# Optimization experiments

Measured on AMD Instinct MI355X. Metric: run time of the kernel, lower is better.

The kernel has to match this reference:

```python
import jax, jax.numpy as jnp
import numpy as np

N_LAYERS = 2
D_MODEL = 768
D_INNER = 1536
D_STATE = 16
D_CONV = 4
DT_RANK = 48
VOCAB = 50257
EPS = 1e-5


def _rms(x, w):
    return x * jax.lax.rsqrt(jnp.mean(x * x, axis=-1, keepdims=True) + EPS) * w


def _mixer(x, in_w, cw, cb, xp_w, dt_w, dt_b, a_log, d_skip, out_w):
    b, l, _ = x.shape
    xz = x @ in_w.T                                  # (b,l,2*d_in)
    u, z = jnp.split(xz, 2, axis=-1)                 # each (b,l,d_in)
    # causal depthwise conv1d
    uc = jax.lax.conv_general_dilated(
        u.transpose(0, 2, 1), cw[:, None, :], (1,), [(D_CONV - 1, 0)],
        feature_group_count=D_INNER, dimension_numbers=("NCH", "OIH", "NCH"))
    u = jax.nn.silu((uc + cb[:, None]).transpose(0, 2, 1))
    x_dbl = u @ xp_w.T                               # (b,l,dt_rank+2n)
    dt, B, C = jnp.split(x_dbl, [DT_RANK, DT_RANK + D_STATE], axis=-1)
    delta = jax.nn.softplus(dt @ dt_w.T + dt_b)      # (b,l,d_in)
    A = -jnp.exp(a_log)                              # (d_in,n)
    dA = jnp.exp(delta[..., None] * A)               # (b,l,d_in,n)
    dBu = delta[..., None] * B[:, :, None, :] * u[..., None]

    def step(h, inp):
        dA_t, dBu_t, C_t = inp
        h = dA_t * h + dBu_t
        return h, jnp.einsum("bdn,bn->bd", h, C_t)

    h0 = jnp.zeros((b, D_INNER, D_STATE), x.dtype)
    _, ys = jax.lax.scan(step, h0, (dA.transpose(1, 0, 2, 3),
                                    dBu.transpose(1, 0, 2, 3),
                                    C.transpose(1, 0, 2)))
    y = ys.transpose(1, 0, 2) + u * d_skip           # (b,l,d_in)
    y = y * jax.nn.silu(z)
    return y @ out_w.T


def setup_inputs() -> dict:
    key = jax.random.key(0)
    ks = jax.random.split(key, 12)
    std = 0.02
    emb = jax.random.normal(ks[0], (VOCAB, D_MODEL), jnp.float32) * std
    emb = emb.at[0].set(0.0)  # padding_idx=0
    tokens = jax.random.randint(ks[1], (2, 1024), 0, VOCAB)
    a_log = jnp.tile(jnp.log(jnp.arange(1, D_STATE + 1, dtype=jnp.float32)),
                     (N_LAYERS, D_INNER, 1))
    return {
        "tokens": tokens,
        "emb": emb,
        "norm_w": jnp.ones((N_LAYERS, D_MODEL), jnp.float32),
        "in_proj_w": jax.random.normal(ks[2], (N_LAYERS, 2 * D_INNER, D_MODEL), jnp.float32) * std,
        "conv_w": jax.random.normal(ks[3], (N_LAYERS, D_INNER, D_CONV), jnp.float32) * 0.1,
        "conv_b": jnp.zeros((N_LAYERS, D_INNER), jnp.float32),
        "x_proj_w": jax.random.normal(ks[4], (N_LAYERS, DT_RANK + 2 * D_STATE, D_INNER), jnp.float32) * std,
        "dt_proj_w": jax.random.normal(ks[5], (N_LAYERS, D_INNER, DT_RANK), jnp.float32) * (DT_RANK ** -0.5),
        "dt_proj_b": jax.random.uniform(ks[6], (N_LAYERS, D_INNER), jnp.float32, -4.6, -2.0),
        "A_log": a_log,
        "D": jnp.ones((N_LAYERS, D_INNER), jnp.float32),
        "out_proj_w": jax.random.normal(ks[7], (N_LAYERS, D_MODEL, D_INNER), jnp.float32) * (std / np.sqrt(2 * N_LAYERS)),
        "normf_w": jnp.ones((D_MODEL,), jnp.float32),
        "lm_head_w": jax.random.normal(ks[8], (VOCAB, D_MODEL), jnp.float32) * std,
    }


def reference(tokens, emb, norm_w, in_proj_w, conv_w, conv_b, x_proj_w,
              dt_proj_w, dt_proj_b, A_log, D, out_proj_w, normf_w, lm_head_w):
    x = emb[tokens]                                  # (b,l,d_model)
    for i in range(N_LAYERS):
        x = x + _mixer(_rms(x, norm_w[i]), in_proj_w[i], conv_w[i], conv_b[i],
                       x_proj_w[i], dt_proj_w[i], dt_proj_b[i], A_log[i],
                       D[i], out_proj_w[i])
    x = _rms(x, normf_w)
    return x @ lm_head_w.T                           # (b,l,vocab)
```

## Files before the change

### kernel.cpp

```cpp
#include <hip/hip_runtime.h>
#include <hip/hip_bf16.h>
#include <math.h>

#define DM 768
#define DI 1536
#define DSN 16
#define NB 2
#define SL 1024
#define MROWS 2048
#define VOC 50257
#define VOCP 50432
#define EPSR 1e-5f

typedef __attribute__((ext_vector_type(8))) short short8;
typedef __attribute__((ext_vector_type(4))) float f32x4;
typedef __attribute__((ext_vector_type(4))) unsigned short us4;
typedef unsigned short u16;

__device__ inline u16 f2bf(float f) {
    unsigned u = __builtin_bit_cast(unsigned, f);
    u += 0x7FFFu + ((u >> 16) & 1u);
    return (u16)(u >> 16);
}

#define G_LDS16(g, l) __builtin_amdgcn_global_load_lds( \
    (const __attribute__((address_space(1))) void*)(g), \
    (__attribute__((address_space(3))) void*)(l), 16, 0, 0)

__global__ __launch_bounds__(256)
void k_embed_rms(const int* __restrict__ tok, const float* __restrict__ emb,
                 const float* __restrict__ w, float* __restrict__ x,
                 u16* __restrict__ out) {
    int r = blockIdx.x;
    int t = tok[r];
    const float* src = emb + (size_t)t * DM;
    int c0 = threadIdx.x * 3;
    float v[3]; float ss = 0.f;
#pragma unroll
    for (int i = 0; i < 3; ++i) {
        v[i] = src[c0 + i]; ss += v[i] * v[i];
        x[(size_t)r * DM + c0 + i] = v[i];
    }
#pragma unroll
    for (int o = 32; o > 0; o >>= 1) ss += __shfl_down(ss, o);
    __shared__ float s[4];
    int lane = threadIdx.x & 63, wv = threadIdx.x >> 6;
    if (lane == 0) s[wv] = ss;
    __syncthreads();
    float sc = rsqrtf((s[0] + s[1] + s[2] + s[3]) / (float)DM + EPSR);
#pragma unroll
    for (int i = 0; i < 3; ++i)
        out[(size_t)r * DM + c0 + i] = f2bf(v[i] * sc * w[c0 + i]);
}

__global__ __launch_bounds__(256)
void k_rmsnorm_bf16(const float* __restrict__ x, const float* __restrict__ w,
                    u16* __restrict__ out) {
    int r = blockIdx.x;
    const float* row = x + (size_t)r * DM;
    int c0 = threadIdx.x * 3;
    float v[3]; float ss = 0.f;
#pragma unroll
    for (int i = 0; i < 3; ++i) { v[i] = row[c0 + i]; ss += v[i] * v[i]; }
#pragma unroll
    for (int o = 32; o > 0; o >>= 1) ss += __shfl_down(ss, o);
    __shared__ float s[4];
    int lane = threadIdx.x & 63, wv = threadIdx.x >> 6;
    if (lane == 0) s[wv] = ss;
    __syncthreads();
    float sc = rsqrtf((s[0] + s[1] + s[2] + s[3]) / (float)DM + EPSR);
#pragma unroll
    for (int i = 0; i < 3; ++i)
        out[(size_t)r * DM + c0 + i] = f2bf(v[i] * sc * w[c0 + i]);
}

struct CvtSeg { const float* src; u16* dst; int sr, sc, sld, dc, blk0, total4; };
struct CvtArgs { CvtSeg seg[9]; };

__global__ __launch_bounds__(256)
void k_cvt_multi(CvtArgs a) {
    int b = blockIdx.x;
    int s = 0;
#pragma unroll
    for (int q = 1; q < 9; ++q) if (a.seg[q].blk0 <= b) s = q;
    const CvtSeg& g = a.seg[s];
    long i4 = (long)(b - g.blk0) * 256 + threadIdx.x;
    if (i4 >= g.total4) return;
    long i = i4 * 4;
    int r = (int)(i / g.dc), c0 = (int)(i % g.dc);
    us4 o;
#pragma unroll
    for (int e = 0; e < 4; ++e) {
        int c = c0 + e;
        float v = (r < g.sr && c < g.sc) ? g.src[(size_t)r * g.sld + c] : 0.f;
        o[e] = f2bf(v);
    }
    *(us4*)&g.dst[i] = o;
}

__global__ void k_cvt_pad4(const float* __restrict__ src, u16* __restrict__ dst,
                           int sr, int sc, int sld, int dc, long total4) {
    long i4 = (long)blockIdx.x * 256 + threadIdx.x;
    if (i4 >= total4) return;
    long i = i4 * 4;
    int r = (int)(i / dc), c0 = (int)(i % dc);
    us4 o;
#pragma unroll
    for (int e = 0; e < 4; ++e) {
        int c = c0 + e;
        float v = (r < sr && c < sc) ? src[(size_t)r * sld + c] : 0.f;
        o[e] = f2bf(v);
    }
    *(us4*)&dst[i] = o;
}

__global__ void k_conv_silu(const float* __restrict__ xz, const float* __restrict__ cw,
                            const float* __restrict__ cb, float* __restrict__ uc,
                            u16* __restrict__ ucb) {
    int d = blockIdx.x * 256 + threadIdx.x;
    int r = blockIdx.y;
    int l = r & (SL - 1);
    float acc = cb[d];
#pragma unroll
    for (int j = 0; j < 4; ++j) {
        int ls = l - 3 + j;
        if (ls >= 0) acc += xz[(size_t)(r - 3 + j) * (2 * DI) + d] * cw[d * 4 + j];
    }
    float s = acc / (1.f + __expf(-acc));
    uc[(size_t)r * DI + d] = s;
    ucb[(size_t)r * DI + d] = f2bf(s);
}

__global__ __launch_bounds__(512)
void k_scan2(const float* __restrict__ delta, const float* __restrict__ uc,
             const float* __restrict__ xdbl, const float* __restrict__ xz,
             const float* __restrict__ alog, const float* __restrict__ Dp,
             u16* __restrict__ ybf) {
    __shared__ float ds2[8][16][20], us2[8][16][20], bn2[8][16][20], cn2[8][16][20];
    __shared__ float Sm[8][16][16], Pm[8][16][16];
    int b  = blockIdx.x / 96;
    int d0 = (blockIdx.x % 96) * 16;
    int tid = threadIdx.x, w = tid >> 6, lane = tid & 63;
    int ch = lane >> 2, nq = lane & 3;
    int d = d0 + ch;
    float A[4];
#pragma unroll
    for (int k = 0; k < 4; ++k) A[k] = -__expf(alog[d * DSN + nq + 4 * k]);
    int tb = w * 128;

    float h[4] = {0.f, 0.f, 0.f, 0.f};
    float sdl = 0.f;
    for (int t0 = 0; t0 < 128; t0 += 16) {
        int row0 = b * SL + tb + t0;
#pragma unroll
        for (int i = 0; i < 4; ++i) {
            int lin = i * 64 + lane, tt = lin >> 4, cc = lin & 15;
            size_t row = (size_t)(row0 + tt);
            ds2[w][cc][tt] = delta[row * DI + d0 + cc];
            us2[w][cc][tt] = uc[row * DI + d0 + cc];
            bn2[w][cc][tt] = xdbl[row * 128 + 48 + cc];
        }
#pragma unroll
        for (int g4 = 0; g4 < 4; ++g4) {
            f32x4 dl = *(const f32x4*)&ds2[w][ch][g4 * 4];
            f32x4 uv = *(const f32x4*)&us2[w][ch][g4 * 4];
            f32x4 bv[4];
#pragma unroll
            for (int k = 0; k < 4; ++k) bv[k] = *(const f32x4*)&bn2[w][nq + 4 * k][g4 * 4];
#pragma unroll
            for (int s = 0; s < 4; ++s) {
                float du = dl[s] * uv[s];
                sdl += dl[s];
#pragma unroll
                for (int k = 0; k < 4; ++k) {
                    float dA = __expf(dl[s] * A[k]);
                    h[k] = h[k] * dA + du * bv[k][s];
                }
            }
        }
    }
#pragma unroll
    for (int k = 0; k < 4; ++k) {
        Sm[w][ch][nq + 4 * k] = h[k];
        Pm[w][ch][nq + 4 * k] = __expf(A[k] * sdl);
    }
    __syncthreads();
    if (tid < 256) {
        int c2 = tid >> 4, n2 = tid & 15;
        float H = 0.f;
#pragma unroll
        for (int g = 0; g < 8; ++g) {
            float hi = H;
            H = Pm[g][c2][n2] * H + Sm[g][c2][n2];
            Sm[g][c2][n2] = hi;
        }
    }
    __syncthreads();
    float Dv = Dp[d];
#pragma unroll
    for (int k = 0; k < 4; ++k) h[k] = Sm[w][ch][nq + 4 * k];
    for (int t0 = 0; t0 < 128; t0 += 16) {
        int row0 = b * SL + tb + t0;
#pragma unroll
        for (int i = 0; i < 4; ++i) {
            int lin = i * 64 + lane, tt = lin >> 4, cc = lin & 15;
            size_t row = (size_t)(row0 + tt);
            ds2[w][cc][tt] = delta[row * DI + d0 + cc];
            us2[w][cc][tt] = uc[row * DI + d0 + cc];
            bn2[w][cc][tt] = xdbl[row * 128 + 48 + cc];
            cn2[w][cc][tt] = xdbl[row * 128 + 64 + cc];
        }
#pragma unroll
        for (int g4 = 0; g4 < 4; ++g4) {
            f32x4 dl = *(const f32x4*)&ds2[w][ch][g4 * 4];
            f32x4 uv = *(const f32x4*)&us2[w][ch][g4 * 4];
            f32x4 bv[4], cv[4];
#pragma unroll
            for (int k = 0; k < 4; ++k) {
                bv[k] = *(const f32x4*)&bn2[w][nq + 4 * k][g4 * 4];
                cv[k] = *(const f32x4*)&cn2[w][nq + 4 * k][g4 * 4];
            }
#pragma unroll
            for (int s = 0; s < 4; ++s) {
                float du = dl[s] * uv[s];
                float p = 0.f;
#pragma unroll
                for (int k = 0; k < 4; ++k) {
                    float dA = __expf(dl[s] * A[k]);
                    h[k] = h[k] * dA + du * bv[k][s];
                    p += h[k] * cv[k][s];
                }
                p += __shfl_xor(p, 1);
                p += __shfl_xor(p, 2);
                if (nq == 0) {
                    size_t row = (size_t)(row0 + g4 * 4 + s);
                    float z = xz[row * (2 * DI) + DI + d];
                    float y = p + uv[s] * Dv;
                    y *= z / (1.f + __expf(-z));
                    ybf[row * DI + d] = f2bf(y);
                }
            }
        }
    }
}

template <int EPIL>
__global__ __launch_bounds__(256)
void k_gemm_bt(const u16* __restrict__ A, const u16* __restrict__ W,
               float* C, const float* RES,
               const float* __restrict__ BIASV,
               int K, int ldc, int nTm) {
    __shared__ u16 Al[128 * 32];
    __shared__ u16 Wl[128 * 32];
    int nwg = gridDim.x;
    int qc = nwg >> 3, rc = nwg & 7;
    int xcd = blockIdx.x & 7, j = blockIdx.x >> 3;
    int wg = (xcd < rc ? xcd * (qc + 1) : rc * (qc + 1) + (xcd - rc) * qc) + j;
    int m0 = (wg % nTm) * 128, n0 = (wg / nTm) * 128;

    int tid = threadIdx.x, wave = tid >> 6, lane = tid & 63;
    int wm = wave >> 1, wn = wave & 1;
    f32x4 acc[4][4] = {};
    const int rS = (lane >> 2);
    const int kS = (((lane & 3) ^ ((lane >> 3) & 3)) * 8);
    const int kofs = (((lane >> 4) ^ ((lane >> 1) & 3)) * 8);
    const int fr = lane & 15;

    for (int k0 = 0; k0 < K; k0 += 32) {
#pragma unroll
        for (int i = 0; i < 2; ++i) {
            int rowA = m0 + wave * 32 + i * 16 + rS;
            G_LDS16(A + (size_t)rowA * K + k0 + kS, &Al[wave * 1024 + i * 512]);
            int rowW = n0 + wave * 32 + i * 16 + rS;
            G_LDS16(W + (size_t)rowW * K + k0 + kS, &Wl[wave * 1024 + i * 512]);
        }
        __syncthreads();
        short8 af[4], bfr[4];
#pragma unroll
        for (int f = 0; f < 4; ++f) {
            af[f]  = *(const short8*)&Al[(wm * 64 + f * 16 + fr) * 32 + kofs];
            bfr[f] = *(const short8*)&Wl[(wn * 64 + f * 16 + fr) * 32 + kofs];
        }
#pragma unroll
        for (int i = 0; i < 4; ++i)
#pragma unroll
            for (int jj = 0; jj < 4; ++jj)
                acc[i][jj] = __builtin_amdgcn_mfma_f32_16x16x32_bf16(af[i], bfr[jj], acc[i][jj], 0, 0, 0);
        __syncthreads();
    }
    int r4 = (lane >> 4) * 4;
#pragma unroll
    for (int i = 0; i < 4; ++i)
#pragma unroll
        for (int jj = 0; jj < 4; ++jj) {
            int col = n0 + wn * 64 + jj * 16 + fr;
            float bia = (EPIL == 2) ? BIASV[col] : 0.f;
#pragma unroll
            for (int rr = 0; rr < 4; ++rr) {
                int row = m0 + wm * 64 + i * 16 + r4 + rr;
                size_t off = (size_t)row * ldc + col;
                float v = acc[i][jj][rr];
                if (EPIL == 1) v += RES[off];
                if (EPIL == 2) { v += bia; v = (v > 20.f) ? v : log1pf(__expf(v)); }
                C[off] = v;
            }
        }
}

#define BAR  __builtin_amdgcn_s_barrier()
#define LGK0 do { asm volatile("s_waitcnt lgkmcnt(0)" ::: "memory"); \
                  __builtin_amdgcn_sched_barrier(0); } while (0)
#define VMC3 asm volatile("s_waitcnt vmcnt(3)" ::: "memory")
#define VMC0 asm volatile("s_waitcnt vmcnt(0)" ::: "memory")

#define STAGE1(t, op, half, GB, RB) do {                                      \
    const u16* _g = (GB) + (size_t)((RB) + (half) * 128 + (w << 4) + srow) * K \
                    + (t) * 32 + scol;                                         \
    G_LDS16(_g, &lds[(t) & 1][op][half][w << 9]);                              \
} while (0)

#define RDA(dst, t, mq) do {                                                   \
    _Pragma("unroll") for (int _m = 0; _m < 4; ++_m)                           \
        dst[_m] = *(const short8*)&lds[(t) & 1][0][wm]                         \
            [((mq) * 64 + _m * 16 + fr) * 32 + rd_sw];                         \
} while (0)

#define RDB(t, nq) do {                                                       \
    _Pragma("unroll") for (int _n = 0; _n < 2; ++_n)                           \
        bfv[_n] = *(const short8*)&lds[(t) & 1][1][wbh]                        \
            [(wbr * 64 + (nq) * 32 + _n * 16 + fr) * 32 + rd_sw];              \
} while (0)

#define MM8(AF, mq, nq) do {                                                  \
    __builtin_amdgcn_s_setprio(1);                                            \
    _Pragma("unroll") for (int _m = 0; _m < 4; ++_m)                           \
    _Pragma("unroll") for (int _n = 0; _n < 2; ++_n)                           \
        acc[(mq) * 4 + _m][(nq) * 2 + _n] =                                    \
            __builtin_amdgcn_mfma_f32_16x16x32_bf16(                           \
                AF[_m], bfv[_n], acc[(mq) * 4 + _m][(nq) * 2 + _n], 0, 0, 0);  \
    __builtin_amdgcn_s_setprio(0);                                            \
} while (0)

template <int K>
__global__ __launch_bounds__(512, 2)
void k_gemm256(const u16* __restrict__ Ap, const u16* __restrict__ Wp,
               float* __restrict__ C, int ldc, int nmax, int nTm) {
    constexpr int NT = K / 32;
    constexpr int NI = NT / 2;
    __shared__ __align__(16) u16 lds[2][2][2][4096];

    int per8 = gridDim.x >> 3;
    int wg = (blockIdx.x & 7) * per8 + (blockIdx.x >> 3);
    int m0 = (wg % nTm) * 256, n0 = (wg / nTm) * 256;

    int tid = threadIdx.x, w = tid >> 6, lane = tid & 63;
    int wm = w >> 2, wn = w & 3, wbh = wn >> 1, wbr = wn & 1;
    int fr = lane & 15;
    int rd_sw = (((lane >> 4) ^ ((lane >> 1) & 3)) * 8);
    int srow  = lane >> 2;
    int scol  = (((lane & 3) ^ ((lane >> 3) & 3)) * 8);

    f32x4 acc[8][4] = {};
    short8 af0[4], af1[4], bfv[2];

    STAGE1(0, 0, 0, Ap, m0); STAGE1(0, 0, 1, Ap, m0);
    STAGE1(0, 1, 0, Wp, n0); STAGE1(0, 1, 1, Wp, n0);
    STAGE1(1, 0, 0, Ap, m0); STAGE1(1, 0, 1, Ap, m0);
    STAGE1(1, 1, 0, Wp, n0);
    VMC3; BAR;

    for (int i = 0; i < NI - 1; ++i) {
        const int ta = 2 * i, tb = 2 * i + 1;
        RDA(af0, ta, 0); RDB(ta, 0);
        STAGE1(tb, 1, 1, Wp, n0);
        BAR; LGK0; MM8(af0, 0, 0); BAR;
        RDA(af1, ta, 1);
        STAGE1(ta + 2, 0, 0, Ap, m0);
        BAR; LGK0; MM8(af1, 1, 0); BAR;
        RDB(ta, 1);
        STAGE1(ta + 2, 0, 1, Ap, m0);
        BAR; LGK0; MM8(af1, 1, 1); BAR;
        STAGE1(ta + 2, 1, 0, Wp, n0);
        BAR; MM8(af0, 0, 1); VMC3; BAR;
        RDA(af0, tb, 0); RDB(tb, 0);
        STAGE1(ta + 2, 1, 1, Wp, n0);
        BAR; LGK0; MM8(af0, 0, 0); BAR;
        RDA(af1, tb, 1);
        STAGE1(ta + 3, 0, 0, Ap, m0);
        BAR; LGK0; MM8(af1, 1, 0); BAR;
        RDB(tb, 1);
        STAGE1(ta + 3, 0, 1, Ap, m0);
        BAR; LGK0; MM8(af1, 1, 1); BAR;
        STAGE1(ta + 3, 1, 0, Wp, n0);
        BAR; MM8(af0, 0, 1); VMC3; BAR;
    }
    {
        const int ta = NT - 2, tb = NT - 1;
        RDA(af0, ta, 0); RDB(ta, 0);
        STAGE1(tb, 1, 1, Wp, n0);
        BAR; LGK0; MM8(af0, 0, 0); BAR;
        RDA(af1, ta, 1);
        BAR; LGK0; MM8(af1, 1, 0); BAR;
        RDB(ta, 1);
        BAR; LGK0; MM8(af1, 1, 1); BAR;
        BAR; MM8(af0, 0, 1); VMC0; BAR;
        RDA(af0, tb, 0); RDB(tb, 0);
        BAR; LGK0; MM8(af0, 0, 0); BAR;
        RDA(af1, tb, 1);
        BAR; LGK0; MM8(af1, 1, 0); BAR;
        RDB(tb, 1);
        BAR; LGK0; MM8(af1, 1, 1); BAR;
        BAR; MM8(af0, 0, 1); BAR;
    }

    int r4 = (lane >> 4) * 4;
#pragma unroll
    for (int mi = 0; mi < 8; ++mi)
#pragma unroll
        for (int ni = 0; ni < 4; ++ni) {
            int col = n0 + wn * 64 + (ni >> 1) * 32 + (ni & 1) * 16 + fr;
            if (col >= nmax) continue;
            int row = m0 + wm * 128 + (mi >> 2) * 64 + (mi & 3) * 16 + r4;
#pragma unroll
            for (int rr = 0; rr < 4; ++rr)
                C[(size_t)(row + rr) * ldc + col] = acc[mi][ni][rr];
        }
}

extern "C" void kernel_launch(void* const* d_in, const int* in_sizes, int n_in,
                              void* d_out, int out_size, void* d_ws, size_t ws_size,
                              hipStream_t stream) {
    (void)in_sizes; (void)n_in; (void)out_size;
    const int*   tok   = (const int*)d_in[0];
    const float* emb   = (const float*)d_in[1];
    const float* normw = (const float*)d_in[2];
    const float* inw   = (const float*)d_in[3];
    const float* cw    = (const float*)d_in[4];
    const float* cb    = (const float*)d_in[5];
    const float* xpw   = (const float*)d_in[6];
    const float* dtw   = (const float*)d_in[7];
    const float* dtb   = (const float*)d_in[8];
    const float* alog  = (const float*)d_in[9];
    const float* Dp    = (const float*)d_in[10];
    const float* outw  = (const float*)d_in[11];
    const float* normf = (const float*)d_in[12];
    const float* lmw   = (const float*)d_in[13];
    float* out = (float*)d_out;

    char* p = (char*)d_ws;
    auto alloc = [&](size_t bytes) { char* r = p; p += (bytes + 255) & ~(size_t)255; return r; };
    float* x     = (float*)alloc((size_t)MROWS * DM * 4);
    u16*   xnb   = (u16*)  alloc((size_t)MROWS * DM * 2);
    float* xz    = (float*)alloc((size_t)MROWS * 2 * DI * 4);
    float* uc    = (float*)alloc((size_t)MROWS * DI * 4);
    u16*   ucb   = (u16*)  alloc((size_t)MROWS * DI * 2);
    float* xdbl  = (float*)alloc((size_t)MROWS * 128 * 4);
    u16*   xdblb = (u16*)  alloc((size_t)MROWS * 64 * 2);
    float* delta = (float*)alloc((size_t)MROWS * DI * 4);
    u16*   ybf   = (u16*)  alloc((size_t)MROWS * DI * 2);
    u16*   winb  = (u16*)  alloc((size_t)NB * (2 * DI) * DM * 2);
    u16*   wxpb  = (u16*)  alloc((size_t)NB * 128 * DI * 2);
    u16*   wdtb  = (u16*)  alloc((size_t)NB * DI * 64 * 2);
    u16*   woutb = (u16*)  alloc((size_t)NB * DM * DI * 2);
    u16*   wlmb  = (u16*)  alloc((size_t)VOCP * DM * 2);
    if ((size_t)(p - (char*)d_ws) > ws_size) return;

    CvtArgs ca;
    int blk = 0;
    auto seg = [&](int idx, const float* s, u16* d, int sr, int sc, int sld, int dc, int dr) {
        int t4 = dr * dc / 4;
        ca.seg[idx] = CvtSeg{s, d, sr, sc, sld, dc, blk, t4};
        blk += (t4 + 255) / 256;
    };
    seg(0, lmw, wlmb, VOC, DM, DM, DM, VOCP);
    seg(1, inw,                          winb,                          2 * DI, DM, DM, DM, 2 * DI);
    seg(2, inw + (size_t)2 * DI * DM,    winb + (size_t)2 * DI * DM,    2 * DI, DM, DM, DM, 2 * DI);
    seg(3, xpw,                          wxpb,                          80, DI, DI, DI, 128);
    seg(4, xpw + (size_t)80 * DI,        wxpb + (size_t)128 * DI,       80, DI, DI, DI, 128);
    seg(5, dtw,                          wdtb,                          DI, 48, 48, 64, DI);
    seg(6, dtw + (size_t)DI * 48,        wdtb + (size_t)DI * 64,        DI, 48, 48, 64, DI);
    seg(7, outw,                         woutb,                         DM, DI, DI, DI, DM);
    seg(8, outw + (size_t)DM * DI,       woutb + (size_t)DM * DI,       DM, DI, DI, DI, DM);
    k_cvt_multi<<<dim3(blk), 256, 0, stream>>>(ca);

    k_embed_rms<<<MROWS, 256, 0, stream>>>(tok, emb, normw, x, xnb);

    for (int i = 0; i < NB; ++i) {
        if (i > 0)
            k_rmsnorm_bf16<<<MROWS, 256, 0, stream>>>(x, normw + i * DM, xnb);

        k_gemm_bt<0><<<dim3(16 * (2 * DI / 128)), 256, 0, stream>>>(
            xnb, winb + (size_t)i * 2 * DI * DM, xz, nullptr, nullptr, DM, 2 * DI, 16);

        k_conv_silu<<<dim3(DI / 256, MROWS), 256, 0, stream>>>(
            xz, cw + (size_t)i * DI * 4, cb + (size_t)i * DI, uc, ucb);

        k_gemm_bt<0><<<dim3(16 * 1), 256, 0, stream>>>(
            ucb, wxpb + (size_t)i * 128 * DI, xdbl, nullptr, nullptr, DI, 128, 16);

        { long t4 = (long)MROWS * 64 / 4;
          k_cvt_pad4<<<dim3((unsigned)((t4 + 255) / 256)), 256, 0, stream>>>(
              xdbl, xdblb, MROWS, 64, 128, 64, t4); }

        k_gemm_bt<2><<<dim3(16 * (DI / 128)), 256, 0, stream>>>(
            xdblb, wdtb + (size_t)i * DI * 64, delta, nullptr, dtb + (size_t)i * DI,
            64, DI, 16);

        k_scan2<<<dim3(NB * (DI / 16)), 512, 0, stream>>>(
            delta, uc, xdbl, xz, alog + (size_t)i * DI * DSN, Dp + i * DI, ybf);

        k_gemm_bt<1><<<dim3(16 * (DM / 128)), 256, 0, stream>>>(
            ybf, woutb + (size_t)i * DM * DI, x, x, nullptr, DI, DM, 16);
    }

    k_rmsnorm_bf16<<<MROWS, 256, 0, stream>>>(x, normf, xnb);
    k_gemm256<DM><<<dim3(8 * (VOCP / 256)), 512, 0, stream>>>(
        xnb, wlmb, out, VOC, VOC, 8);
}
```

Measured before the change: 794.3 us.

## Split-K the x_proj GEMM with a fused reduce/convert, and merge LM-head MFMA phases

The x_proj GEMM (N=128, K=1536) ran on only 16 workgroups. It is now split 8 ways along K into a partial buffer, and a new reduction kernel sums the partials and writes both the fp32 and bf16 copies, which replaces the separate pad/convert kernel. Separately, the LM-head GEMM main loop now issues both A-fragment LDS reads up front and runs two MFMA groups between each barrier pair, roughly halving its barriers. The costs are an extra 8 MB partial buffer round trip and higher register pressure in the LM-head kernel.

```diff
diff --git a/kernel.cpp b/kernel.cpp
--- a/kernel.cpp
+++ b/kernel.cpp
@@ -98,22 +98,6 @@
     *(us4*)&g.dst[i] = o;
 }
 
-__global__ void k_cvt_pad4(const float* __restrict__ src, u16* __restrict__ dst,
-                           int sr, int sc, int sld, int dc, long total4) {
-    long i4 = (long)blockIdx.x * 256 + threadIdx.x;
-    if (i4 >= total4) return;
-    long i = i4 * 4;
-    int r = (int)(i / dc), c0 = (int)(i % dc);
-    us4 o;
-#pragma unroll
-    for (int e = 0; e < 4; ++e) {
-        int c = c0 + e;
-        float v = (r < sr && c < sc) ? src[(size_t)r * sld + c] : 0.f;
-        o[e] = f2bf(v);
-    }
-    *(us4*)&dst[i] = o;
-}
-
 __global__ void k_conv_silu(const float* __restrict__ xz, const float* __restrict__ cw,
                             const float* __restrict__ cb, float* __restrict__ uc,
                             u16* __restrict__ ucb) {
@@ -129,6 +113,19 @@
     float s = acc / (1.f + __expf(-acc));
     uc[(size_t)r * DI + d] = s;
     ucb[(size_t)r * DI + d] = f2bf(s);
+}
+
+__global__ __launch_bounds__(256)
+void k_xp_red(const float* __restrict__ part, float* __restrict__ xdbl,
+              u16* __restrict__ xdblb) {
+    int idx = blockIdx.x * 256 + threadIdx.x;
+    int row = idx >> 7, col = idx & 127;
+    const float* p = part + (size_t)row * 1024 + col;
+    float s = 0.f;
+#pragma unroll
+    for (int k = 0; k < 8; ++k) s += p[k * 128];
+    xdbl[(size_t)row * 128 + col] = s;
+    if (col < 64) xdblb[(size_t)row * 64 + col] = f2bf(s);
 }
 
 __global__ __launch_bounds__(512)
@@ -244,19 +241,23 @@
     }
 }
 
-template <int EPIL>
+template <int EPIL, bool SPLITK>
 __global__ __launch_bounds__(256)
 void k_gemm_bt(const u16* __restrict__ A, const u16* __restrict__ W,
                float* C, const float* RES,
                const float* __restrict__ BIASV,
-               int K, int ldc, int nTm) {
+               int K, int ldk, int ldc, int nTm) {
     __shared__ u16 Al[128 * 32];
     __shared__ u16 Wl[128 * 32];
     int nwg = gridDim.x;
     int qc = nwg >> 3, rc = nwg & 7;
     int xcd = blockIdx.x & 7, j = blockIdx.x >> 3;
     int wg = (xcd < rc ? xcd * (qc + 1) : rc * (qc + 1) + (xcd - rc) * qc) + j;
-    int m0 = (wg % nTm) * 128, n0 = (wg / nTm) * 128;
+    int m0 = (wg % nTm) * 128;
+    int sl = wg / nTm;
+    int n0 = SPLITK ? 0 : sl * 128;
+    int cb = SPLITK ? sl * 128 : n0;
+    int kb = SPLITK ? sl * K : 0;
 
     int tid = threadIdx.x, wave = tid >> 6, lane = tid & 63;
     int wm = wave >> 1, wn = wave & 1;
@@ -270,9 +271,9 @@
 #pragma unroll
         for (int i = 0; i < 2; ++i) {
             int rowA = m0 + wave * 32 + i * 16 + rS;
-            G_LDS16(A + (size_t)rowA * K + k0 + kS, &Al[wave * 1024 + i * 512]);
+            G_LDS16(A + (size_t)rowA * ldk + kb + k0 + kS, &Al[wave * 1024 + i * 512]);
             int rowW = n0 + wave * 32 + i * 16 + rS;
-            G_LDS16(W + (size_t)rowW * K + k0 + kS, &Wl[wave * 1024 + i * 512]);
+            G_LDS16(W + (size_t)rowW * ldk + kb + k0 + kS, &Wl[wave * 1024 + i * 512]);
         }
         __syncthreads();
         short8 af[4], bfr[4];
@@ -293,7 +294,7 @@
     for (int i = 0; i < 4; ++i)
 #pragma unroll
         for (int jj = 0; jj < 4; ++jj) {
-            int col = n0 + wn * 64 + jj * 16 + fr;
+            int col = cb + wn * 64 + jj * 16 + fr;
             float bia = (EPIL == 2) ? BIASV[col] : 0.f;
 #pragma unroll
             for (int rr = 0; rr < 4; ++rr) {
@@ -371,46 +372,34 @@
 
     for (int i = 0; i < NI - 1; ++i) {
         const int ta = 2 * i, tb = 2 * i + 1;
-        RDA(af0, ta, 0); RDB(ta, 0);
+        RDA(af0, ta, 0); RDA(af1, ta, 1); RDB(ta, 0);
         STAGE1(tb, 1, 1, Wp, n0);
-        BAR; LGK0; MM8(af0, 0, 0); BAR;
-        RDA(af1, ta, 1);
         STAGE1(ta + 2, 0, 0, Ap, m0);
-        BAR; LGK0; MM8(af1, 1, 0); BAR;
+        BAR; LGK0; MM8(af0, 0, 0); MM8(af1, 1, 0); BAR;
         RDB(ta, 1);
         STAGE1(ta + 2, 0, 1, Ap, m0);
-        BAR; LGK0; MM8(af1, 1, 1); BAR;
         STAGE1(ta + 2, 1, 0, Wp, n0);
-        BAR; MM8(af0, 0, 1); VMC3; BAR;
-        RDA(af0, tb, 0); RDB(tb, 0);
+        BAR; LGK0; MM8(af1, 1, 1); MM8(af0, 0, 1); VMC3; BAR;
+        RDA(af0, tb, 0); RDA(af1, tb, 1); RDB(tb, 0);
         STAGE1(ta + 2, 1, 1, Wp, n0);
-        BAR; LGK0; MM8(af0, 0, 0); BAR;
-        RDA(af1, tb, 1);
         STAGE1(ta + 3, 0, 0, Ap, m0);
-        BAR; LGK0; MM8(af1, 1, 0); BAR;
+        BAR; LGK0; MM8(af0, 0, 0); MM8(af1, 1, 0); BAR;
         RDB(tb, 1);
         STAGE1(ta + 3, 0, 1, Ap, m0);
-        BAR; LGK0; MM8(af1, 1, 1); BAR;
         STAGE1(ta + 3, 1, 0, Wp, n0);
-        BAR; MM8(af0, 0, 1); VMC3; BAR;
+        BAR; LGK0; MM8(af1, 1, 1); MM8(af0, 0, 1); VMC3; BAR;
     }
     {
         const int ta = NT - 2, tb = NT - 1;
-        RDA(af0, ta, 0); RDB(ta, 0);
+        RDA(af0, ta, 0); RDA(af1, ta, 1); RDB(ta, 0);
         STAGE1(tb, 1, 1, Wp, n0);
-        BAR; LGK0; MM8(af0, 0, 0); BAR;
-        RDA(af1, ta, 1);
-        BAR; LGK0; MM8(af1, 1, 0); BAR;
+        BAR; LGK0; MM8(af0, 0, 0); MM8(af1, 1, 0); BAR;
         RDB(ta, 1);
-        BAR; LGK0; MM8(af1, 1, 1); BAR;
-        BAR; MM8(af0, 0, 1); VMC0; BAR;
-        RDA(af0, tb, 0); RDB(tb, 0);
-        BAR; LGK0; MM8(af0, 0, 0); BAR;
-        RDA(af1, tb, 1);
-        BAR; LGK0; MM8(af1, 1, 0); BAR;
+        BAR; LGK0; MM8(af1, 1, 1); MM8(af0, 0, 1); VMC0; BAR;
+        RDA(af0, tb, 0); RDA(af1, tb, 1); RDB(tb, 0);
+        BAR; LGK0; MM8(af0, 0, 0); MM8(af1, 1, 0); BAR;
         RDB(tb, 1);
-        BAR; LGK0; MM8(af1, 1, 1); BAR;
-        BAR; MM8(af0, 0, 1); BAR;
+        BAR; LGK0; MM8(af1, 1, 1); MM8(af0, 0, 1); BAR;
     }
 
     int r4 = (lane >> 4) * 4;
@@ -456,6 +445,7 @@
     u16*   ucb   = (u16*)  alloc((size_t)MROWS * DI * 2);
     float* xdbl  = (float*)alloc((size_t)MROWS * 128 * 4);
     u16*   xdblb = (u16*)  alloc((size_t)MROWS * 64 * 2);
+    float* part  = (float*)alloc((size_t)MROWS * 1024 * 4);
     float* delta = (float*)alloc((size_t)MROWS * DI * 4);
     u16*   ybf   = (u16*)  alloc((size_t)MROWS * DI * 2);
     u16*   winb  = (u16*)  alloc((size_t)NB * (2 * DI) * DM * 2);
@@ -489,28 +479,27 @@
         if (i > 0)
             k_rmsnorm_bf16<<<MROWS, 256, 0, stream>>>(x, normw + i * DM, xnb);
 
-        k_gemm_bt<0><<<dim3(16 * (2 * DI / 128)), 256, 0, stream>>>(
-            xnb, winb + (size_t)i * 2 * DI * DM, xz, nullptr, nullptr, DM, 2 * DI, 16);
+        k_gemm_bt<0, false><<<dim3(16 * (2 * DI / 128)), 256, 0, stream>>>(
+            xnb, winb + (size_t)i * 2 * DI * DM, xz, nullptr, nullptr,
+            DM, DM, 2 * DI, 16);
 
         k_conv_silu<<<dim3(DI / 256, MROWS), 256, 0, stream>>>(
             xz, cw + (size_t)i * DI * 4, cb + (size_t)i * DI, uc, ucb);
 
-        k_gemm_bt<0><<<dim3(16 * 1), 256, 0, stream>>>(
-            ucb, wxpb + (size_t)i * 128 * DI, xdbl, nullptr, nullptr, DI, 128, 16);
-
-        { long t4 = (long)MROWS * 64 / 4;
-          k_cvt_pad4<<<dim3((unsigned)((t4 + 255) / 256)), 256, 0, stream>>>(
-              xdbl, xdblb, MROWS, 64, 128, 64, t4); }
-
-        k_gemm_bt<2><<<dim3(16 * (DI / 128)), 256, 0, stream>>>(
+        k_gemm_bt<0, true><<<dim3(16 * 8), 256, 0, stream>>>(
+            ucb, wxpb + (size_t)i * 128 * DI, part, nullptr, nullptr,
+            DI / 8, DI, 1024, 16);
+        k_xp_red<<<dim3(MROWS * 128 / 256), 256, 0, stream>>>(part, xdbl, xdblb);
+
+        k_gemm_bt<2, false><<<dim3(16 * (DI / 128)), 256, 0, stream>>>(
             xdblb, wdtb + (size_t)i * DI * 64, delta, nullptr, dtb + (size_t)i * DI,
-            64, DI, 16);
+            64, 64, DI, 16);
 
         k_scan2<<<dim3(NB * (DI / 16)), 512, 0, stream>>>(
             delta, uc, xdbl, xz, alog + (size_t)i * DI * DSN, Dp + i * DI, ybf);
 
-        k_gemm_bt<1><<<dim3(16 * (DM / 128)), 256, 0, stream>>>(
-            ybf, woutb + (size_t)i * DM * DI, x, x, nullptr, DI, DM, 16);
+        k_gemm_bt<1, false><<<dim3(16 * (DM / 128)), 256, 0, stream>>>(
+            ybf, woutb + (size_t)i * DM * DI, x, x, nullptr, DI, DI, DM, 16);
     }
 
     k_rmsnorm_bf16<<<MROWS, 256, 0, stream>>>(x, normf, xnb);
```

New measurement: 747.7 us. 5.9% less time.
